# Kernel optimization log

Hardware: AMD Instinct MI355X
Metric: run time of the kernel (lower is better)

Reference implementation:

```python
import jax, jax.numpy as jnp
import numpy as np

H, W = 4096, 4096
MIN_VAL, MAX_VAL = 0, 256
D = MAX_VAL - MIN_VAL - 1  # 255 candidate thresholds t = 0..254
N_BINS = MAX_VAL           # pixel values live in [0, 256)


def setup_inputs() -> dict:
    key = jax.random.key(0)
    img = jax.random.randint(key, (H, W), MIN_VAL, MAX_VAL, dtype=jnp.int32)
    return {"img_HxW": img}


def reference(img_HxW):
    hw = H * W
    flat = img_HxW.ravel()
    # Histogram of pixel counts and pixel-value sums (float32 accumulation,
    # matching torch.sum(..., dtype=torch.float32) in the original).
    cnt = jax.ops.segment_sum(jnp.ones_like(flat, jnp.float32), flat, num_segments=N_BINS)
    val_sum = jax.ops.segment_sum(flat.astype(jnp.float32), flat, num_segments=N_BINS)
    # Cumulative sums give, for each threshold t, the count/sum of pixels <= t.
    # This equals the original's broadcast compare + masked sum over [H*W, d].
    num_b = jnp.cumsum(cnt)[:D]        # pixels in class "black" (<= t)
    sum_b = jnp.cumsum(val_sum)[:D]    # sum of those pixels
    num_w = hw - num_b                  # pixels in class "white" (> t)
    sum_w = jnp.sum(val_sum) - sum_b
    mean_b = sum_b / num_b
    mean_w = sum_w / num_w
    var_hist = num_b * num_w * (mean_b - mean_w) ** 2  # inter-class variance
    thresh = jnp.argmax(var_hist).astype(jnp.int32)
    bin_img = jnp.where(img_HxW <= thresh,
                        jnp.int32(MIN_VAL), jnp.int32(MAX_VAL))
    return thresh, bin_img
```

## Files before the change

### kernel.cpp

```cpp
#include <hip/hip_runtime.h>

#define HW_TOTAL (4096 * 4096)
#define NBINS 256
#define NCHUNK (HW_TOTAL / 4)
#define HIST_B 512
#define BLK 1024
#define BATCH 8

typedef int int4n __attribute__((ext_vector_type(4)));

#define WS_NEED (HIST_B * NBINS * 4 + 256)

template <int MODE>
__global__ __launch_bounds__(BLK, 8) void otsu_hist_k(const int4* __restrict__ img4,
                                                      unsigned* __restrict__ out) {
    __shared__ unsigned h[4 * NBINS];
    const int t = threadIdx.x;
    for (int i = t; i < 4 * NBINS; i += BLK) h[i] = 0;
    __syncthreads();

    const unsigned sub = (unsigned)t & 3u;
    const int i0 = blockIdx.x * (BLK * BATCH) + t;
    int4 v[BATCH];
#pragma unroll
    for (int k = 0; k < BATCH; ++k) v[k] = img4[i0 + k * BLK];
#pragma unroll
    for (int k = 0; k < BATCH; ++k) {
        atomicAdd(&h[(((unsigned)v[k].x) << 2) | sub], 1u);
        atomicAdd(&h[(((unsigned)v[k].y) << 2) | sub], 1u);
        atomicAdd(&h[(((unsigned)v[k].z) << 2) | sub], 1u);
        atomicAdd(&h[(((unsigned)v[k].w) << 2) | sub], 1u);
    }
    __syncthreads();

    if (t < NBINS) {
        unsigned s = h[t << 2] + h[(t << 2) | 1] + h[(t << 2) | 2] + h[(t << 2) | 3];
        if (MODE == 0) {
            out[blockIdx.x * NBINS + t] = s;
        } else {
            if (s) atomicAdd(&out[t], s);
        }
    }
}

__global__ __launch_bounds__(1024) void otsu_thresh_k(const unsigned* __restrict__ partials,
                                                      int B,
                                                      int* __restrict__ d_out,
                                                      int* __restrict__ thresh_ws) {
    __shared__ unsigned red[4][NBINS];
    __shared__ unsigned cnt[NBINS];

    const int bin = threadIdx.x & 255;
    const int q = threadIdx.x >> 8;
    const int BQ = (B + 3) / 4;
    int r = q * BQ;
    const int e = min((q + 1) * BQ, B);
    unsigned s = 0;
    for (; r + 8 <= e; r += 8) {
#pragma unroll
        for (int k = 0; k < 8; ++k) s += partials[(r + k) * NBINS + bin];
    }
    for (; r < e; ++r) s += partials[r * NBINS + bin];
    red[q][bin] = s;
    __syncthreads();

    if (threadIdx.x < NBINS)
        cnt[bin] = red[0][bin] + red[1][bin] + red[2][bin] + red[3][bin];
    __syncthreads();

    if (threadIdx.x >= 64) return;
    const int lane = threadIdx.x;

    uint4 c4 = ((const uint4*)cnt)[lane];
    unsigned cs[4] = {c4.x, c4.y, c4.z, c4.w};

    unsigned long long lc[4], lv[4];
    unsigned long long ccum = 0ull, vcum = 0ull;
#pragma unroll
    for (int k = 0; k < 4; ++k) {
        ccum += cs[k];
        vcum += (unsigned long long)cs[k] * (unsigned)(4 * lane + k);
        lc[k] = ccum;
        lv[k] = vcum;
    }
    unsigned long long cscan = ccum, vscan = vcum;
    for (int d = 1; d < 64; d <<= 1) {
        unsigned long long cu = __shfl_up(cscan, d);
        unsigned long long vu = __shfl_up(vscan, d);
        if (lane >= d) { cscan += cu; vscan += vu; }
    }
    const unsigned long long cbase = cscan - ccum;
    const unsigned long long vbase = vscan - vcum;
    const unsigned long long vtotal = __shfl(vscan, 63);

    double best = -1.0;
    int bestt = 255;
    const double hw = (double)HW_TOTAL;
    const double vtot_d = (double)vtotal;
#pragma unroll
    for (int k = 0; k < 4; ++k) {
        int tt = 4 * lane + k;
        if (tt > 254) continue;
        double nb = (double)(cbase + lc[k]);
        double sb = (double)(vbase + lv[k]);
        double nw = hw - nb;
        double sw = vtot_d - sb;
        double dm = sb / nb - sw / nw;
        double var = nb * nw * dm * dm;
        if (var > best || (var == best && tt < bestt)) { best = var; bestt = tt; }
    }
    for (int d = 32; d >= 1; d >>= 1) {
        double ov = __shfl_xor(best, d);
        int ot = __shfl_xor(bestt, d);
        if (ov > best || (ov == best && ot < bestt)) { best = ov; bestt = ot; }
    }
    if (lane == 0) {
        d_out[0] = bestt;
        *thresh_ws = bestt;
    }
}

__global__ __launch_bounds__(BLK, 8) void otsu_bin_k(const int* __restrict__ img,
                                                     int* __restrict__ out,
                                                     const int* __restrict__ thresh_ws) {
    const int thresh = *thresh_ws;
    const int t = threadIdx.x;
    const int lane = t & 63;
    const int i0 = blockIdx.x * (BLK * BATCH) + t;
    const int4* img4 = (const int4*)img;
#pragma unroll
    for (int k = 0; k < BATCH; ++k) {
        const int c = i0 + k * BLK;
        int4 v = img4[c];
        int prev = __shfl_up(v.w, 1);
        if (lane == 0) prev = (c > 0) ? img[4 * c - 1] : 0;
        int4n o;
        o.x = (c == 0) ? thresh : ((prev <= thresh) ? 0 : 256);
        o.y = (v.x <= thresh) ? 0 : 256;
        o.z = (v.y <= thresh) ? 0 : 256;
        o.w = (v.z <= thresh) ? 0 : 256;
        __builtin_nontemporal_store(o, (int4n*)out + c);
    }
    if (blockIdx.x == 0 && t == 0)
        out[HW_TOTAL] = (img[HW_TOTAL - 1] <= thresh) ? 0 : 256;
}

extern "C" void kernel_launch(void* const* d_in, const int* in_sizes, int n_in,
                              void* d_out, int out_size, void* d_ws, size_t ws_size,
                              hipStream_t stream) {
    const int* img = (const int*)d_in[0];
    int* out = (int*)d_out;
    int* thresh_ws = (int*)d_ws;
    unsigned* hist_buf = (unsigned*)((char*)d_ws + 256);

    if (ws_size >= (size_t)WS_NEED) {
        otsu_hist_k<0><<<HIST_B, BLK, 0, stream>>>((const int4*)img, hist_buf);
        otsu_thresh_k<<<1, 1024, 0, stream>>>(hist_buf, HIST_B, out, thresh_ws);
    } else {
        (void)hipMemsetAsync(hist_buf, 0, NBINS * sizeof(unsigned), stream);
        otsu_hist_k<1><<<HIST_B, BLK, 0, stream>>>((const int4*)img, hist_buf);
        otsu_thresh_k<<<1, 1024, 0, stream>>>(hist_buf, 1, out, thresh_ws);
    }
    otsu_bin_k<<<HIST_B, BLK, 0, stream>>>(img, out, thresh_ws);
}
```

Before: 45.82 us.

## Use per-wave contiguous chunks and unaligned shifted loads in the binarize kernel

The histogram and binarize kernels now give each wave a contiguous range of int4 chunks instead of striding by the block size. The binarize kernel drops the cross-lane shuffle and the extra scalar load for the shifted output and reads one unaligned 4-int vector starting one element earlier. Its output store becomes a regular store instead of a nontemporal one. The threshold kernel's partial-histogram reduction is unrolled 16-wide instead of 8. Unaligned vector loads can cross cache-line boundaries and split into extra transactions, and removing the nontemporal hint changes how the output interacts with the cache.

```diff
diff --git a/kernel.cpp b/kernel.cpp
--- a/kernel.cpp
+++ b/kernel.cpp
@@ -8,6 +8,7 @@
 #define BATCH 8
 
 typedef int int4n __attribute__((ext_vector_type(4)));
+typedef int int4a __attribute__((ext_vector_type(4), aligned(4)));
 
 #define WS_NEED (HIST_B * NBINS * 4 + 256)
 
@@ -19,17 +20,19 @@
     for (int i = t; i < 4 * NBINS; i += BLK) h[i] = 0;
     __syncthreads();
 
-    const unsigned sub = (unsigned)t & 3u;
-    const int i0 = blockIdx.x * (BLK * BATCH) + t;
+    unsigned* hp = h + (t & 3);
+    const int wave = t >> 6, lane = t & 63;
+    const int i0 = blockIdx.x * (BLK * BATCH) + wave * (64 * BATCH) + lane;
+
     int4 v[BATCH];
 #pragma unroll
-    for (int k = 0; k < BATCH; ++k) v[k] = img4[i0 + k * BLK];
+    for (int k = 0; k < BATCH; ++k) v[k] = img4[i0 + k * 64];
 #pragma unroll
     for (int k = 0; k < BATCH; ++k) {
-        atomicAdd(&h[(((unsigned)v[k].x) << 2) | sub], 1u);
-        atomicAdd(&h[(((unsigned)v[k].y) << 2) | sub], 1u);
-        atomicAdd(&h[(((unsigned)v[k].z) << 2) | sub], 1u);
-        atomicAdd(&h[(((unsigned)v[k].w) << 2) | sub], 1u);
+        atomicAdd(&hp[((unsigned)v[k].x) << 2], 1u);
+        atomicAdd(&hp[((unsigned)v[k].y) << 2], 1u);
+        atomicAdd(&hp[((unsigned)v[k].z) << 2], 1u);
+        atomicAdd(&hp[((unsigned)v[k].w) << 2], 1u);
     }
     __syncthreads();
 
@@ -56,9 +59,9 @@
     int r = q * BQ;
     const int e = min((q + 1) * BQ, B);
     unsigned s = 0;
-    for (; r + 8 <= e; r += 8) {
+    for (; r + 16 <= e; r += 16) {
 #pragma unroll
-        for (int k = 0; k < 8; ++k) s += partials[(r + k) * NBINS + bin];
+        for (int k = 0; k < 16; ++k) s += partials[(r + k) * NBINS + bin];
     }
     for (; r < e; ++r) s += partials[r * NBINS + bin];
     red[q][bin] = s;
@@ -125,23 +128,25 @@
                                                      const int* __restrict__ thresh_ws) {
     const int thresh = *thresh_ws;
     const int t = threadIdx.x;
-    const int lane = t & 63;
-    const int i0 = blockIdx.x * (BLK * BATCH) + t;
-    const int4* img4 = (const int4*)img;
+    const int wave = t >> 6, lane = t & 63;
+    const int i0 = blockIdx.x * (BLK * BATCH) + wave * (64 * BATCH) + lane;
+
 #pragma unroll
     for (int k = 0; k < BATCH; ++k) {
-        const int c = i0 + k * BLK;
-        int4 v = img4[c];
-        int prev = __shfl_up(v.w, 1);
-        if (lane == 0) prev = (c > 0) ? img[4 * c - 1] : 0;
+        const int c = i0 + k * 64;
+        const int4a* vp = (const int4a*)(img + (c ? 4 * c - 1 : 0));
+        int4a v = *vp;
         int4n o;
-        o.x = (c == 0) ? thresh : ((prev <= thresh) ? 0 : 256);
-        o.y = (v.x <= thresh) ? 0 : 256;
-        o.z = (v.y <= thresh) ? 0 : 256;
-        o.w = (v.z <= thresh) ? 0 : 256;
-        __builtin_nontemporal_store(o, (int4n*)out + c);
+        o.x = (v.x <= thresh) ? 0 : 256;
+        o.y = (v.y <= thresh) ? 0 : 256;
+        o.z = (v.z <= thresh) ? 0 : 256;
+        o.w = (v.w <= thresh) ? 0 : 256;
+        if (c == 0) {
+            o.w = o.z; o.z = o.y; o.y = o.x; o.x = thresh;
+        }
+        *((int4n*)out + c) = o;
     }
-    if (blockIdx.x == 0 && t == 0)
+    if (i0 == 0)
         out[HW_TOTAL] = (img[HW_TOTAL - 1] <= thresh) ? 0 : 256;
 }
 
```

Measured after the change: 44.24 us. 1.04x faster.
